# Performance work log

Hardware: AMD Instinct MI355X
Metric: run time of the kernel (lower is better)

## Reference

```python
import jax, jax.numpy as jnp
import numpy as np

B, L, D, H, DFF, MODES, ELAYERS = 64, 512, 512, 8, 2048, 32, 2
VOCAB, NUM_APP, KERNEL = 10000, 10000, 25
E = D // H


def setup_inputs() -> dict:
    key = jax.random.key(0)
    ks = jax.random.split(key, 16)
    scale = 1.0 / (D * D)  # FourierBlock weight init scale
    return {
        'x_app': jax.random.randint(ks[0], (B, L), 0, VOCAB),
        'x_time': jax.random.uniform(ks[1], (B, L), dtype=jnp.float32),
        'time_vecs': jax.random.normal(ks[2], (B, L, 24), dtype=jnp.float32),
        'targets': jax.random.randint(ks[3], (B,), 0, NUM_APP),
        'app_emb_w': jax.random.normal(ks[4], (VOCAB, D), dtype=jnp.float32) * 0.02,
        'time_w': jax.random.normal(ks[5], (D,), dtype=jnp.float32) * 0.02,
        'time_b': jnp.zeros((D,), jnp.float32),
        'Wq': jax.random.normal(ks[6], (ELAYERS, D, D), dtype=jnp.float32) * 0.02,
        'bq': jnp.zeros((ELAYERS, D), jnp.float32),
        'Wo': jax.random.normal(ks[7], (ELAYERS, D, D), dtype=jnp.float32) * 0.02,
        'bo': jnp.zeros((ELAYERS, D), jnp.float32),
        'four_wr': jax.random.uniform(ks[8], (ELAYERS, H, E, E, MODES), dtype=jnp.float32) * scale,
        'four_wi': jax.random.uniform(ks[9], (ELAYERS, H, E, E, MODES), dtype=jnp.float32) * scale,
        'conv1_w': jax.random.normal(ks[10], (ELAYERS, DFF, D), dtype=jnp.float32) * 0.02,
        'conv2_w': jax.random.normal(ks[11], (ELAYERS, D, DFF), dtype=jnp.float32) * 0.02,
        'norm_w': jnp.ones((D,), jnp.float32),
        'norm_b': jnp.zeros((D,), jnp.float32),
        'proj_w': jax.random.normal(ks[12], (NUM_APP, D + 24), dtype=jnp.float32) * 0.02,
        'proj_b': jnp.zeros((NUM_APP,), jnp.float32),
    }


def moving_avg(x):
    # edge-replicate pad by (K-1)//2 on each side, then AvgPool1d(K, stride=1)
    pad = (KERNEL - 1) // 2
    xp = jnp.pad(x, ((0, 0), (pad, pad), (0, 0)), mode='edge')  # [B, L+K-1, D]
    cs = jnp.cumsum(xp, axis=1)
    cs = jnp.concatenate([jnp.zeros_like(cs[:, :1]), cs], axis=1)
    return (cs[:, KERNEL:] - cs[:, :-KERNEL]) / KERNEL  # [B, L, D]


def series_decomp(x):
    m = moving_avg(x)
    return x - m, m


def my_layernorm(x, w, b, eps=1e-5):
    mu = jnp.mean(x, axis=-1, keepdims=True)
    var = jnp.mean((x - mu) ** 2, axis=-1, keepdims=True)
    xh = (x - mu) * jax.lax.rsqrt(var + eps) * w + b
    # my_Layernorm: subtract per-sample mean over the sequence dim
    return xh - jnp.mean(xh, axis=1, keepdims=True)


def fourier_block(q, wr, wi):
    # q: [B, L, H, E] -> [B, H, E, L]
    Bq, Lq, Hq, Eq = q.shape
    x = jnp.transpose(q, (0, 2, 3, 1))
    x_ft = jnp.fft.rfft(x, axis=-1)             # [B,H,E,L//2+1] complex64
    xs = x_ft[..., :MODES]                      # low-frequency mode selection
    w = (wr + 1j * wi).astype(xs.dtype)         # [H,E,E,M]
    out_sel = jnp.einsum('bhim,hiom->bhom', xs, w)
    out_ft = jnp.zeros((Bq, Hq, Eq, Lq // 2 + 1), dtype=xs.dtype).at[..., :MODES].set(out_sel)
    return jnp.fft.irfft(out_ft, n=Lq, axis=-1)  # [B,H,E,L]


def encoder_layer(x, Wq, bq, Wo, bo, wr, wi, c1, c2):
    Bx, Lx, Dx = x.shape
    q = (x @ Wq.T + bq).reshape(Bx, Lx, H, E)
    out = fourier_block(q, wr, wi)               # [B,H,E,L]
    # faithful to torch: out.view(B, L, -1) is a raw row-major reinterpret
    out = out.reshape(Bx, Lx, H * E)
    new_x = out @ Wo.T + bo
    x = x + new_x
    x, _ = series_decomp(x)
    y = jax.nn.relu(jnp.einsum('bld,fd->blf', x, c1))   # conv1 (1x1, no bias)
    y = jnp.einsum('blf,df->bld', y, c2)                # conv2 (1x1, no bias)
    res, _ = series_decomp(x + y)
    return res


def reference(x_app, x_time, time_vecs, targets, app_emb_w, time_w, time_b,
              Wq, bq, Wo, bo, four_wr, four_wi, conv1_w, conv2_w,
              norm_w, norm_b, proj_w, proj_b):
    x = app_emb_w[x_app] + x_time[..., None] * time_w + time_b  # [B,L,D]
    for l in range(ELAYERS):
        x = encoder_layer(x, Wq[l], bq[l], Wo[l], bo[l],
                          four_wr[l], four_wi[l], conv1_w[l], conv2_w[l])
    x = my_layernorm(x, norm_w, norm_b)
    last = x[:, -1, :]                                   # [B,D]
    out = jnp.concatenate([last, time_vecs[:, -1, :]], axis=1)  # [B,D+24]
    score = out @ proj_w.T + proj_b                      # [B,NUM_APP]
    return score  # mode='predict' returns score
```

## Files before the change

### kernel.cpp

```cpp
#include <hip/hip_runtime.h>


typedef unsigned short u16;
typedef float f32x4 __attribute__((ext_vector_type(4)));
typedef __bf16 bf16x8 __attribute__((ext_vector_type(8)));

__device__ __forceinline__ u16 f2b(float f) {
  unsigned u = __float_as_uint(f);
  return (u16)((u + 0x7FFFu + ((u >> 16) & 1u)) >> 16);
}
__device__ __forceinline__ float b2f(u16 v) {
  return __uint_as_float((unsigned)v << 16);
}
__device__ __forceinline__ f32x4 b4f(ushort4 v) {
  f32x4 r;
  r.x = b2f(v.x); r.y = b2f(v.y); r.z = b2f(v.z); r.w = b2f(v.w);
  return r;
}

__device__ __forceinline__ void gll16(const void* g, void* l) {
  __builtin_amdgcn_global_load_lds(
      (const __attribute__((address_space(1))) void*)g,
      (__attribute__((address_space(3))) void*)l, 16, 0, 0);
}

template<bool SWAP>
__device__ __forceinline__ f32x4 mfma16(bf16x8 a, bf16x8 b, f32x4 c) {
  if constexpr (SWAP)
    return __builtin_amdgcn_mfma_f32_16x16x32_bf16(b, a, c, 0, 0, 0);
  else
    return __builtin_amdgcn_mfma_f32_16x16x32_bf16(a, b, c, 0, 0, 0);
}

template<bool BIAS, bool RELU, bool RES, bool OUTBF16, bool GUARD, bool TRANS,
         bool SWZ>
__global__ __launch_bounds__(256, 3)
void k_gemm(const u16* __restrict__ A, const u16* __restrict__ B,
            const float* __restrict__ bias, const u16* __restrict__ res,
            float* __restrict__ Cf, u16* __restrict__ Cb,
            int M, int N, int K,
            long zA, long zB, long zC, int nbn, int nbm)
{
  __shared__ __align__(16) u16 sA[2][128 * 32];
  __shared__ __align__(16) u16 sB[2][128 * 32];
  const int tid = threadIdx.x;
  const int wave = tid >> 6, lane = tid & 63;
  int bn, bm;
  if (SWZ) {
    int bid = blockIdx.x;
    int xcd = bid & 7, loc = bid >> 3;
    bn = loc % nbn;
    bm = xcd * (nbm >> 3) + loc / nbn;
  } else {
    bn = blockIdx.x;
    bm = blockIdx.y;
  }
  const int bz = blockIdx.z;
  const int wm = (wave >> 1) * 64, wn = (wave & 1) * 64;

  A += (size_t)bz * zA;
  B += (size_t)bz * zB;

  const int r0 = tid >> 2;
  const int lg = tid & 3;
  const int ps = lg ^ ((r0 >> 1) & 3);
  int gmA0 = bm * 128 + r0, gmA1 = gmA0 + 64;
  int gnB0 = bn * 128 + r0, gnB1 = gnB0 + 64;
  if (GUARD) {
    gmA0 = gmA0 < M ? gmA0 : M - 1;
    gmA1 = gmA1 < M ? gmA1 : M - 1;
    gnB0 = gnB0 < N ? gnB0 : N - 1;
    gnB1 = gnB1 < N ? gnB1 : N - 1;
  }
  const size_t rb = (size_t)K * 2;
  const char* pa0 = (const char*)A + (size_t)gmA0 * rb + lg * 16;
  const char* pa1 = (const char*)A + (size_t)gmA1 * rb + lg * 16;
  const char* pb0 = (const char*)B + (size_t)gnB0 * rb + lg * 16;
  const char* pb1 = (const char*)B + (size_t)gnB1 * rb + lg * 16;
  const int w0 = r0 * 32 + ps * 8;

  f32x4 acc[4][4];
  const f32x4 z = {0.f, 0.f, 0.f, 0.f};
#pragma unroll
  for (int i = 0; i < 4; ++i)
#pragma unroll
    for (int j = 0; j < 4; ++j) acc[i][j] = z;

  const int r = lane & 15, qd = lane >> 4;
  const int pA = (qd ^ ((lane >> 1) & 3)) * 8;
  const int nk = K >> 5;

  uint4 va0, va1, vb0, vb1;
  auto gload = [&](int kt) {
    const size_t ko = (size_t)kt * 64;
    va0 = *(const uint4*)(pa0 + ko);
    va1 = *(const uint4*)(pa1 + ko);
    vb0 = *(const uint4*)(pb0 + ko);
    vb1 = *(const uint4*)(pb1 + ko);
  };

  gload(0);
  int pg = 0;
  for (int kt = 0; kt < nk; ++kt) {
    *(uint4*)&sA[pg][w0]        = va0;
    *(uint4*)&sA[pg][w0 + 2048] = va1;
    *(uint4*)&sB[pg][w0]        = vb0;
    *(uint4*)&sB[pg][w0 + 2048] = vb1;
    if (kt + 1 < nk) gload(kt + 1);
    __syncthreads();
    bf16x8 af[4], bg[4];
#pragma unroll
    for (int mi = 0; mi < 4; ++mi)
      af[mi] = *(const bf16x8*)&sA[pg][(wm + mi * 16 + r) * 32 + pA];
#pragma unroll
    for (int ni = 0; ni < 4; ++ni)
      bg[ni] = *(const bf16x8*)&sB[pg][(wn + ni * 16 + r) * 32 + pA];
#pragma unroll
    for (int mi = 0; mi < 4; ++mi)
#pragma unroll
      for (int ni = 0; ni < 4; ++ni)
        acc[mi][ni] = mfma16<!TRANS>(af[mi], bg[ni], acc[mi][ni]);
    pg ^= 1;
  }

  if (Cf) Cf += (size_t)bz * zC;
  if (Cb) Cb += (size_t)bz * zC;

  if constexpr (!TRANS) {
#pragma unroll
    for (int mi = 0; mi < 4; ++mi) {
      const int gm = bm * 128 + wm + mi * 16 + r;
      if (GUARD && gm >= M) continue;
#pragma unroll
      for (int ni = 0; ni < 4; ++ni) {
        const int gn0 = bn * 128 + wn + ni * 16 + qd * 4;
        if (GUARD && gn0 >= N) continue;
        float v[4];
        ushort4 rv;
        if (RES) rv = *(const ushort4*)&res[(size_t)gm * N + gn0];
#pragma unroll
        for (int e = 0; e < 4; ++e) {
          v[e] = acc[mi][ni][e];
          if (BIAS) v[e] += bias[gn0 + e];
          if (RES)  v[e] += b2f(e == 0 ? rv.x : e == 1 ? rv.y : e == 2 ? rv.z : rv.w);
          if (RELU) v[e] = v[e] > 0.f ? v[e] : 0.f;
        }
        if (OUTBF16) {
          ushort4 o;
          o.x = f2b(v[0]); o.y = f2b(v[1]); o.z = f2b(v[2]); o.w = f2b(v[3]);
          *(ushort4*)&Cb[(size_t)gm * N + gn0] = o;
        } else {
          float4 o = {v[0], v[1], v[2], v[3]};
          *(float4*)&Cf[(size_t)gm * N + gn0] = o;
        }
      }
    }
  } else {
#pragma unroll
    for (int ni = 0; ni < 4; ++ni) {
      const int gn = bn * 128 + wn + ni * 16 + r;
      if (GUARD && gn >= N) continue;
      const float bb = BIAS ? bias[gn] : 0.f;
#pragma unroll
      for (int mi = 0; mi < 4; ++mi) {
        const int gm0 = bm * 128 + wm + mi * 16 + qd * 4;
        if (GUARD && gm0 >= M) continue;
        float v[4];
#pragma unroll
        for (int e = 0; e < 4; ++e) {
          v[e] = acc[mi][ni][e];
          if (BIAS) v[e] += bb;
          if (RELU) v[e] = v[e] > 0.f ? v[e] : 0.f;
        }
        if (OUTBF16) {
          ushort4 o;
          o.x = f2b(v[0]); o.y = f2b(v[1]); o.z = f2b(v[2]); o.w = f2b(v[3]);
          *(ushort4*)&Cb[(size_t)gn * M + gm0] = o;
        } else {
          float4 o = {v[0], v[1], v[2], v[3]};
          *(float4*)&Cf[(size_t)gn * M + gm0] = o;
        }
      }
    }
  }
}

template<bool BIAS, bool RELU, bool RES, bool TRANS>
__global__ __launch_bounds__(512, 4)
void k_gemm3(const u16* __restrict__ A, const u16* __restrict__ B,
             const float* __restrict__ bias, const u16* __restrict__ res,
             u16* __restrict__ C, int M, int N, int K,
             int nbn, int nbm, long zA, long zC)
{
  __shared__ __align__(16) u16 sA[3][256 * 32];
  __shared__ __align__(16) u16 sB[3][128 * 32];
  const int tid = threadIdx.x;
  const int w8 = tid >> 6, lane = tid & 63;
  const int bid = blockIdx.x;
  const int xcd = bid & 7, loc = bid >> 3;
  const int mpx = (int)(gridDim.x >> 3) / nbn;
  const int mflat = xcd * mpx + loc / nbn;
  const int bn = loc % nbn;
  const int bz = mflat / nbm;
  const int bm = mflat - bz * nbm;
  const int wm = (w8 >> 1) * 64, wn = (w8 & 1) * 64;

  A += (size_t)bz * zA;

  const int r0 = tid >> 2;
  const int lg = (tid & 3) ^ ((r0 >> 1) & 3);
  const u16* pA0 = A + (size_t)(bm * 256 + r0) * K + lg * 8;
  const u16* pA1 = pA0 + (size_t)128 * K;
  const u16* pB0 = B + (size_t)(bn * 128 + r0) * K + lg * 8;
  const int la0 = w8 * 512;
  const int la1 = 4096 + w8 * 512;

  const int nk = K >> 5;

  auto stage = [&](int t, int sb) {
    const size_t ko = (size_t)t * 32;
    gll16(pA0 + ko, &sA[sb][0] + la0);
    gll16(pA1 + ko, &sA[sb][0] + la1);
    gll16(pB0 + ko, &sB[sb][0] + la0);
  };

  f32x4 acc[4][4];
  const f32x4 z = {0.f, 0.f, 0.f, 0.f};
#pragma unroll
  for (int i = 0; i < 4; ++i)
#pragma unroll
    for (int j = 0; j < 4; ++j) acc[i][j] = z;

  const int fr = lane & 15, qd = lane >> 4;
  const int pAo = ((qd ^ ((lane >> 1) & 3)) << 3);

  stage(0, 0);
  stage(1, 1);
  int cb = 0;
  for (int t = 0; t < nk; ++t) {
    if (t + 1 < nk) asm volatile("s_waitcnt vmcnt(3)" ::: "memory");
    else            asm volatile("s_waitcnt vmcnt(0)" ::: "memory");
    __builtin_amdgcn_s_barrier();
    asm volatile("" ::: "memory");
    const u16* bufA = &sA[cb][0];
    const u16* bufB = &sB[cb][0];
    bf16x8 af[4], bg[4];
#pragma unroll
    for (int i = 0; i < 4; ++i)
      af[i] = *(const bf16x8*)&bufA[(wm + i * 16 + fr) * 32 + pAo];
#pragma unroll
    for (int i = 0; i < 4; ++i)
      bg[i] = *(const bf16x8*)&bufB[(wn + i * 16 + fr) * 32 + pAo];
    if (t + 2 < nk) {
      int sb = cb + 2; if (sb >= 3) sb -= 3;
      stage(t + 2, sb);
    }
    __builtin_amdgcn_s_setprio(1);
#pragma unroll
    for (int mi = 0; mi < 4; ++mi)
#pragma unroll
      for (int ni = 0; ni < 4; ++ni)
        acc[mi][ni] = mfma16<!TRANS>(af[mi], bg[ni], acc[mi][ni]);
    __builtin_amdgcn_s_setprio(0);
    cb = (cb == 2) ? 0 : cb + 1;
  }

  C += (size_t)bz * zC;

  if constexpr (!TRANS) {
#pragma unroll
    for (int mi = 0; mi < 4; ++mi) {
      const int gm = bm * 256 + wm + mi * 16 + fr;
#pragma unroll
      for (int ni = 0; ni < 4; ++ni) {
        const int gn0 = bn * 128 + wn + ni * 16 + qd * 4;
        float v[4];
        ushort4 rv;
        if (RES) rv = *(const ushort4*)&res[(size_t)gm * N + gn0];
#pragma unroll
        for (int e = 0; e < 4; ++e) {
          v[e] = acc[mi][ni][e];
          if (BIAS) v[e] += bias[gn0 + e];
          if (RES)  v[e] += b2f(e == 0 ? rv.x : e == 1 ? rv.y : e == 2 ? rv.z : rv.w);
          if (RELU) v[e] = v[e] > 0.f ? v[e] : 0.f;
        }
        ushort4 o;
        o.x = f2b(v[0]); o.y = f2b(v[1]); o.z = f2b(v[2]); o.w = f2b(v[3]);
        *(ushort4*)&C[(size_t)gm * N + gn0] = o;
      }
    }
  } else {
#pragma unroll
    for (int ni = 0; ni < 4; ++ni) {
      const int gn = bn * 128 + wn + ni * 16 + fr;
      const float bb = BIAS ? bias[gn] : 0.f;
#pragma unroll
      for (int mi = 0; mi < 4; ++mi) {
        const int gm0 = bm * 256 + wm + mi * 16 + qd * 4;
        float v[4];
#pragma unroll
        for (int e = 0; e < 4; ++e) {
          v[e] = acc[mi][ni][e];
          if (BIAS) v[e] += bb;
          if (RELU) v[e] = v[e] > 0.f ? v[e] : 0.f;
        }
        ushort4 o;
        o.x = f2b(v[0]); o.y = f2b(v[1]); o.z = f2b(v[2]); o.w = f2b(v[3]);
        *(ushort4*)&C[(size_t)gn * M + gm0] = o;
      }
    }
  }
}

__global__ void k_basis(u16* __restrict__ dftB, u16* __restrict__ Binv)
{
  int id = blockIdx.x * 256 + threadIdx.x;
  if (id >= 32768) return;
  {
    int m = id >> 9, l = id & 511;
    int mm = m & 31;
    float ang = (float)((l * mm) & 511) * (6.283185307179586f / 512.f);
    float s, c;
    __sincosf(ang, &s, &c);
    dftB[id] = f2b(m < 32 ? c : -s);
  }
  {
    int l = id >> 6, m = id & 63;
    int mm = m & 31;
    float ang = (float)((l * mm) & 511) * (6.283185307179586f / 512.f);
    float s, c;
    __sincosf(ang, &s, &c);
    float v;
    if (m < 32) v = (m == 0 ? 1.f : 2.f) * (1.f / 512.f) * c;
    else        v = (mm == 0 ? 0.f : (-2.f / 512.f) * s);
    Binv[id] = f2b(v);
  }
}

__global__ void k_convert(const float* __restrict__ in, u16* __restrict__ out, int n)
{
  int id = blockIdx.x * 256 + threadIdx.x;
  if (id < n) out[id] = f2b(in[id]);
}

__global__ void k_convproj(const float* __restrict__ w, u16* __restrict__ o)
{
  int id = blockIdx.x * 256 + threadIdx.x;
  if (id >= 10000 * 544) return;
  int n = id / 544, k = id % 544;
  o[id] = f2b(k < 536 ? w[(size_t)n * 536 + k] : 0.f);
}

__global__ void k_transp(const float* __restrict__ wr, const float* __restrict__ wi,
                         float* __restrict__ wrT, float* __restrict__ wiT)
{
  __shared__ float tr[64 * 33], ti[64 * 33];
  int blk = blockIdx.x;
  int t = threadIdx.x;
  int lh = blk >> 6, i = blk & 63;
  const size_t src = (size_t)blk * 2048;
#pragma unroll
  for (int p = 0; p < 8; ++p) {
    int id = p * 256 + t;
    int o = id >> 5, m = id & 31;
    tr[o * 33 + m] = wr[src + id];
    ti[o * 33 + m] = wi[src + id];
  }
  __syncthreads();
#pragma unroll
  for (int p = 0; p < 8; ++p) {
    int id = p * 256 + t;
    int m = id >> 6, o = id & 63;
    size_t dst = ((size_t)(lh * 32 + m) * 64 + i) * 64 + o;
    wrT[dst] = tr[o * 33 + m];
    wiT[dst] = ti[o * 33 + m];
  }
}

__global__ void k_embed(const int* __restrict__ xapp, const float* __restrict__ xtime,
                        const float* __restrict__ emb, const float* __restrict__ tw,
                        const float* __restrict__ tb, u16* __restrict__ xb)
{
  int id = blockIdx.x * 256 + threadIdx.x;
  int j = id & 127, bl = id >> 7;
  float4 e = ((const float4*)emb)[(size_t)xapp[bl] * 128 + j];
  float t = xtime[bl];
  float4 w4 = ((const float4*)tw)[j];
  float4 b4 = ((const float4*)tb)[j];
  ushort4 o;
  o.x = f2b(e.x + t * w4.x + b4.x);
  o.y = f2b(e.y + t * w4.y + b4.y);
  o.z = f2b(e.z + t * w4.z + b4.z);
  o.w = f2b(e.w + t * w4.w + b4.w);
  ((ushort4*)xb)[id] = o;
}

__global__ __launch_bounds__(256)
void k_mix(const float* __restrict__ spec, const float* __restrict__ wrT,
           const float* __restrict__ wiT, u16* __restrict__ Ab)
{
  __shared__ float swr[4096], swi[4096];
  __shared__ float sre[4][64], sim[4][64];
  int hm = blockIdx.x;
  int bg = blockIdx.y;
  int h = hm >> 5, m = hm & 31, t = threadIdx.x;
  const float* wrb = wrT + (size_t)hm * 4096;
  const float* wib = wiT + (size_t)hm * 4096;
#pragma unroll
  for (int p = 0; p < 16; ++p) {
    int id = p * 256 + t;
    swr[id] = wrb[id];
    swi[id] = wib[id];
  }
  int o = t & 63, bsub = t >> 6;
  for (int b0 = 0; b0 < 16; b0 += 4) {
    __syncthreads();
    int b = bg * 16 + b0 + bsub;
    const float* spb = spec + (size_t)b * 32768;
    sre[bsub][o] = spb[m * 512 + h * 64 + o];
    sim[bsub][o] = spb[(32 + m) * 512 + h * 64 + o];
    __syncthreads();
    float aR = 0.f, aI = 0.f;
#pragma unroll 8
    for (int i = 0; i < 64; ++i) {
      float xr = sre[bsub][i], xi = sim[bsub][i];
      float wrv = swr[i * 64 + o], wiv = swi[i * 64 + o];
      aR += xr * wrv - xi * wiv;
      aI += xr * wiv + xi * wrv;
    }
    size_t row = (size_t)b * 512 + h * 64 + o;
    Ab[row * 64 + m] = f2b(aR);
    Ab[row * 64 + 32 + m] = f2b(aI);
  }
}

__global__ void k_decomp(const u16* __restrict__ in, u16* __restrict__ outb)
{
  int blk = blockIdx.x;
  int j = blk >> 3;
  int b = (blk & 7) + 8 * (j >> 3);
  int ck = (j & 7) * 2 + (threadIdx.x >> 7);
  int d4 = threadIdx.x & 127;
  const ushort4* xb = (const ushort4*)(in + (size_t)b * 262144) + d4;
  ushort4* ob = (ushort4*)(outb + (size_t)b * 262144) + d4;
  int l0 = ck * 32;
  f32x4 sum = {0.f, 0.f, 0.f, 0.f};
#pragma unroll
  for (int jj = -12; jj <= 12; ++jj) {
    int idx = l0 + jj;
    idx = idx < 0 ? 0 : idx;
    sum += b4f(xb[idx * 128]);
  }
#pragma unroll 4
  for (int l = l0; l < l0 + 32; ++l) {
    f32x4 xv = b4f(xb[l * 128]);
    f32x4 o = xv - sum * (1.f / 25.f);
    ushort4 ov;
    ov.x = f2b(o.x); ov.y = f2b(o.y); ov.z = f2b(o.z); ov.w = f2b(o.w);
    ob[l * 128] = ov;
    int ia = l + 13 > 511 ? 511 : l + 13;
    int ir = l - 12 < 0 ? 0 : l - 12;
    sum += b4f(xb[ia * 128]) - b4f(xb[ir * 128]);
  }
}

__global__ void k_lnstats(const u16* __restrict__ x, float* __restrict__ mu,
                          float* __restrict__ rs)
{
  int row = blockIdx.x;
  const u16* xr = x + (size_t)row * 512;
  int t = threadIdx.x;
  ushort2 p = ((const ushort2*)xr)[t];
  float v0 = b2f(p.x), v1 = b2f(p.y);
  float s = v0 + v1, ss = v0 * v0 + v1 * v1;
#pragma unroll
  for (int off = 32; off; off >>= 1) {
    s += __shfl_down(s, off);
    ss += __shfl_down(ss, off);
  }
  __shared__ float as[4], ass[4];
  if ((t & 63) == 0) { as[t >> 6] = s; ass[t >> 6] = ss; }
  __syncthreads();
  if (t == 0) {
    float S = as[0] + as[1] + as[2] + as[3];
    float SS = ass[0] + ass[1] + ass[2] + ass[3];
    float m = S * (1.f / 512.f);
    float var = SS * (1.f / 512.f) - m * m;
    mu[row] = m;
    rs[row] = rsqrtf(var + 1e-5f);
  }
}

__global__ void k_lastcat1(const u16* __restrict__ x, const float* __restrict__ mu,
                           const float* __restrict__ rs, float* __restrict__ part)
{
  int b = blockIdx.x >> 3, g = blockIdx.x & 7, t = threadIdx.x;
  const u16* xb = x + (size_t)b * 262144;
  const float* mub = mu + b * 512;
  const float* rsb = rs + b * 512;
  float a0 = 0.f, a1 = 0.f;
#pragma unroll 4
  for (int l = g * 64; l < g * 64 + 64; ++l) {
    float m = mub[l], rr = rsb[l];
    ushort2 p = ((const ushort2*)(xb + l * 512))[t];
    a0 += (b2f(p.x) - m) * rr;
    a1 += (b2f(p.y) - m) * rr;
  }
  part[((size_t)b * 8 + g) * 512 + 2 * t]     = a0;
  part[((size_t)b * 8 + g) * 512 + 2 * t + 1] = a1;
}

__global__ void k_lastcat2(const u16* __restrict__ x, const float* __restrict__ mu,
                           const float* __restrict__ rs, const float* __restrict__ part,
                           const float* __restrict__ nw, u16* __restrict__ cat)
{
  int b = blockIdx.x, t = threadIdx.x;
#pragma unroll
  for (int hh = 0; hh < 2; ++hh) {
    int d = t + hh * 256;
    float acc = 0.f;
#pragma unroll
    for (int g = 0; g < 8; ++g)
      acc += part[((size_t)b * 8 + g) * 512 + d];
    float lastv = (b2f(x[(size_t)b * 262144 + 511 * 512 + d]) - mu[b * 512 + 511])
                  * rs[b * 512 + 511];
    cat[b * 544 + d] = f2b(nw[d] * (lastv - acc * (1.f / 512.f)));
  }
}

__global__ void k_timecat(const float* __restrict__ tv, u16* __restrict__ cat)
{
  int id = blockIdx.x * 256 + threadIdx.x;
  if (id >= 2048) return;
  int b = id >> 5, j = id & 31;
  int pos = 512 + j;
  float v = (pos < 536) ? tv[((size_t)b * 512 + 511) * 24 + (pos - 512)] : 0.f;
  cat[b * 544 + pos] = f2b(v);
}

extern "C" void kernel_launch(void* const* d_in, const int* in_sizes, int n_in,
                              void* d_out, int out_size, void* d_ws, size_t ws_size,
                              hipStream_t stream)
{
  (void)in_sizes; (void)n_in; (void)out_size; (void)ws_size;
  const int*   x_app  = (const int*)  d_in[0];
  const float* x_time = (const float*)d_in[1];
  const float* tvec   = (const float*)d_in[2];
  const float* emb    = (const float*)d_in[4];
  const float* time_w = (const float*)d_in[5];
  const float* time_b = (const float*)d_in[6];
  const float* Wq     = (const float*)d_in[7];
  const float* bq     = (const float*)d_in[8];
  const float* Wo     = (const float*)d_in[9];
  const float* bo     = (const float*)d_in[10];
  const float* fwr    = (const float*)d_in[11];
  const float* fwi    = (const float*)d_in[12];
  const float* c1     = (const float*)d_in[13];
  const float* c2     = (const float*)d_in[14];
  const float* norm_w = (const float*)d_in[15];
  const float* proj_w = (const float*)d_in[17];
  const float* proj_b = (const float*)d_in[18];
  float* out = (float*)d_out;

  char* w = (char*)d_ws;
  auto alloc = [&](size_t bytes) -> char* {
    char* p = w;
    w += (bytes + 255) & ~(size_t)255;
    return p;
  };
  u16*   Cb   = (u16*)  alloc(33554432);
  u16*   YqT  = (u16*)  alloc(134217728);
  u16*   T1b  = (u16*)  alloc(33554432);
  float* S1   = (float*)alloc(8388608);
  u16*   Coef = (u16*)  alloc(4194304);
  float* wrT  = (float*)alloc(2 * 1048576 * 4);
  float* wiT  = (float*)alloc(2 * 1048576 * 4);
  u16*   wqb  = (u16*)  alloc(2 * 262144 * 2);
  u16*   wob  = (u16*)  alloc(2 * 262144 * 2);
  u16*   c1b  = (u16*)  alloc(2 * 1048576 * 2);
  u16*   c2b  = (u16*)  alloc(2 * 1048576 * 2);
  u16*   pwb  = (u16*)  alloc(10000 * 544 * 2);
  u16*   dftB = (u16*)  alloc(64 * 512 * 2);
  u16*   Binv = (u16*)  alloc(512 * 64 * 2);
  float* muB  = (float*)alloc(131072);
  float* rsB  = (float*)alloc(131072);
  float* part = (float*)alloc(64 * 8 * 512 * 4);
  u16*   cat  = (u16*)  alloc(64 * 544 * 2);

  k_basis<<<128, 256, 0, stream>>>(dftB, Binv);
  k_transp<<<1024, 256, 0, stream>>>(fwr, fwi, wrT, wiT);
  k_convert<<<2048, 256, 0, stream>>>(Wq, wqb, 524288);
  k_convert<<<2048, 256, 0, stream>>>(Wo, wob, 524288);
  k_convert<<<8192, 256, 0, stream>>>(c1, c1b, 2097152);
  k_convert<<<8192, 256, 0, stream>>>(c2, c2b, 2097152);
  k_convproj<<<21250, 256, 0, stream>>>(proj_w, pwb);
  k_embed<<<16384, 256, 0, stream>>>(x_app, x_time, emb, time_w, time_b, Cb);

  for (int l = 0; l < 2; ++l) {
    const u16* wq_l = wqb + l * 262144;
    const u16* wo_l = wob + l * 262144;
    const u16* c1_l = c1b + l * 1048576;
    const u16* c2_l = c2b + l * 1048576;

    k_gemm3<true, false, false, true>
        <<<512, 512, 0, stream>>>(
        Cb, wq_l, bq + l * 512, nullptr, YqT, 512, 512, 512,
        4, 2, 262144, 262144);
    k_gemm<false, false, false, false, true, true, false>
        <<<dim3(1, 4, 64), 256, 0, stream>>>(
        YqT, dftB, nullptr, nullptr, S1, nullptr, 512, 64, 512,
        262144, 0, 32768, 0, 0);
    k_mix<<<dim3(256, 4), 256, 0, stream>>>(
        S1, wrT + l * 1048576, wiT + l * 1048576, Coef);
    k_gemm<false, false, false, true, false, false, true>
        <<<dim3(1024, 1, 1), 256, 0, stream>>>(
        Coef, Binv, nullptr, nullptr, nullptr, YqT, 32768, 512, 64,
        0, 0, 0, 4, 256);
    k_gemm3<true, false, true, false>
        <<<512, 512, 0, stream>>>(
        YqT, wo_l, bo + l * 512, Cb, T1b, 32768, 512, 512,
        4, 128, 0, 0);
    k_decomp<<<512, 256, 0, stream>>>(T1b, Cb);
    k_gemm3<false, true, false, false>
        <<<2048, 512, 0, stream>>>(
        Cb, c1_l, nullptr, nullptr, YqT, 32768, 2048, 512,
        16, 128, 0, 0);
    k_gemm3<false, false, true, false>
        <<<512, 512, 0, stream>>>(
        YqT, c2_l, nullptr, Cb, T1b, 32768, 512, 2048,
        4, 128, 0, 0);
    k_decomp<<<512, 256, 0, stream>>>(T1b, Cb);
  }

  k_lnstats<<<32768, 256, 0, stream>>>(Cb, muB, rsB);
  k_lastcat1<<<512, 256, 0, stream>>>(Cb, muB, rsB, part);
  k_lastcat2<<<64, 256, 0, stream>>>(Cb, muB, rsB, part, norm_w, cat);
  k_timecat<<<8, 256, 0, stream>>>(tvec, cat);
  k_gemm<true, false, false, false, true, false, false>
      <<<dim3(79, 1, 1), 256, 0, stream>>>(
      cat, pwb, proj_b, nullptr, out, nullptr, 64, 10000, 544,
      0, 0, 0, 0, 0);
}
```

Baseline: 872.6 us.

## Use 4-wave GEMM blocks with 128x64 per-wave tiles and double buffering

The bf16 GEMM kernel used for the linear layers now runs 256 threads per block instead of 512, while the 256x128 block tile stays the same. Each wave now computes a 128x64 sub-tile with 32 accumulators instead of 16, which doubles register reuse of the B fragments per LDS read. The LDS pipeline drops from triple to double buffering and waits for all loads before each step, freeing shared memory but leaving less prefetch overlap. The higher register pressure and fewer waves per block may reduce latency hiding.

```diff
diff --git a/kernel.cpp b/kernel.cpp
--- a/kernel.cpp
+++ b/kernel.cpp
@@ -186,16 +186,16 @@
 }
 
 template<bool BIAS, bool RELU, bool RES, bool TRANS>
-__global__ __launch_bounds__(512, 4)
-void k_gemm3(const u16* __restrict__ A, const u16* __restrict__ B,
+__global__ __launch_bounds__(256, 3)
+void k_gemm4(const u16* __restrict__ A, const u16* __restrict__ B,
              const float* __restrict__ bias, const u16* __restrict__ res,
              u16* __restrict__ C, int M, int N, int K,
              int nbn, int nbm, long zA, long zC)
 {
-  __shared__ __align__(16) u16 sA[3][256 * 32];
-  __shared__ __align__(16) u16 sB[3][128 * 32];
+  __shared__ __align__(16) u16 sA[2][256 * 32];
+  __shared__ __align__(16) u16 sB[2][128 * 32];
   const int tid = threadIdx.x;
-  const int w8 = tid >> 6, lane = tid & 63;
+  const int w4 = tid >> 6, lane = tid & 63;
   const int bid = blockIdx.x;
   const int xcd = bid & 7, loc = bid >> 3;
   const int mpx = (int)(gridDim.x >> 3) / nbn;
@@ -203,31 +203,32 @@
   const int bn = loc % nbn;
   const int bz = mflat / nbm;
   const int bm = mflat - bz * nbm;
-  const int wm = (w8 >> 1) * 64, wn = (w8 & 1) * 64;
+  const int wm = (w4 >> 1) * 128, wn = (w4 & 1) * 64;
 
   A += (size_t)bz * zA;
 
   const int r0 = tid >> 2;
   const int lg = (tid & 3) ^ ((r0 >> 1) & 3);
   const u16* pA0 = A + (size_t)(bm * 256 + r0) * K + lg * 8;
-  const u16* pA1 = pA0 + (size_t)128 * K;
   const u16* pB0 = B + (size_t)(bn * 128 + r0) * K + lg * 8;
-  const int la0 = w8 * 512;
-  const int la1 = 4096 + w8 * 512;
+  const int wb = w4 * 512;
 
   const int nk = K >> 5;
 
   auto stage = [&](int t, int sb) {
     const size_t ko = (size_t)t * 32;
-    gll16(pA0 + ko, &sA[sb][0] + la0);
-    gll16(pA1 + ko, &sA[sb][0] + la1);
-    gll16(pB0 + ko, &sB[sb][0] + la0);
+#pragma unroll
+    for (int j = 0; j < 4; ++j)
+      gll16(pA0 + (size_t)(j * 64) * K + ko, &sA[sb][j * 2048 + wb]);
+#pragma unroll
+    for (int j = 0; j < 2; ++j)
+      gll16(pB0 + (size_t)(j * 64) * K + ko, &sB[sb][j * 2048 + wb]);
   };
 
-  f32x4 acc[4][4];
+  f32x4 acc[8][4];
   const f32x4 z = {0.f, 0.f, 0.f, 0.f};
 #pragma unroll
-  for (int i = 0; i < 4; ++i)
+  for (int i = 0; i < 8; ++i)
 #pragma unroll
     for (int j = 0; j < 4; ++j) acc[i][j] = z;
 
@@ -235,41 +236,35 @@
   const int pAo = ((qd ^ ((lane >> 1) & 3)) << 3);
 
   stage(0, 0);
-  stage(1, 1);
-  int cb = 0;
   for (int t = 0; t < nk; ++t) {
-    if (t + 1 < nk) asm volatile("s_waitcnt vmcnt(3)" ::: "memory");
-    else            asm volatile("s_waitcnt vmcnt(0)" ::: "memory");
+    const int cb = t & 1;
+    asm volatile("s_waitcnt vmcnt(0)" ::: "memory");
     __builtin_amdgcn_s_barrier();
     asm volatile("" ::: "memory");
     const u16* bufA = &sA[cb][0];
     const u16* bufB = &sB[cb][0];
-    bf16x8 af[4], bg[4];
-#pragma unroll
-    for (int i = 0; i < 4; ++i)
+    bf16x8 af[8], bg[4];
+#pragma unroll
+    for (int i = 0; i < 8; ++i)
       af[i] = *(const bf16x8*)&bufA[(wm + i * 16 + fr) * 32 + pAo];
 #pragma unroll
     for (int i = 0; i < 4; ++i)
       bg[i] = *(const bf16x8*)&bufB[(wn + i * 16 + fr) * 32 + pAo];
-    if (t + 2 < nk) {
-      int sb = cb + 2; if (sb >= 3) sb -= 3;
-      stage(t + 2, sb);
-    }
+    if (t + 1 < nk) stage(t + 1, cb ^ 1);
     __builtin_amdgcn_s_setprio(1);
 #pragma unroll
-    for (int mi = 0; mi < 4; ++mi)
+    for (int mi = 0; mi < 8; ++mi)
 #pragma unroll
       for (int ni = 0; ni < 4; ++ni)
         acc[mi][ni] = mfma16<!TRANS>(af[mi], bg[ni], acc[mi][ni]);
     __builtin_amdgcn_s_setprio(0);
-    cb = (cb == 2) ? 0 : cb + 1;
   }
 
   C += (size_t)bz * zC;
 
   if constexpr (!TRANS) {
 #pragma unroll
-    for (int mi = 0; mi < 4; ++mi) {
+    for (int mi = 0; mi < 8; ++mi) {
       const int gm = bm * 256 + wm + mi * 16 + fr;
 #pragma unroll
       for (int ni = 0; ni < 4; ++ni) {
@@ -295,7 +290,7 @@
       const int gn = bn * 128 + wn + ni * 16 + fr;
       const float bb = BIAS ? bias[gn] : 0.f;
 #pragma unroll
-      for (int mi = 0; mi < 4; ++mi) {
+      for (int mi = 0; mi < 8; ++mi) {
         const int gm0 = bm * 256 + wm + mi * 16 + qd * 4;
         float v[4];
 #pragma unroll
@@ -602,8 +597,8 @@
     const u16* c1_l = c1b + l * 1048576;
     const u16* c2_l = c2b + l * 1048576;
 
-    k_gemm3<true, false, false, true>
-        <<<512, 512, 0, stream>>>(
+    k_gemm4<true, false, false, true>
+        <<<512, 256, 0, stream>>>(
         Cb, wq_l, bq + l * 512, nullptr, YqT, 512, 512, 512,
         4, 2, 262144, 262144);
     k_gemm<false, false, false, false, true, true, false>
@@ -616,17 +611,17 @@
         <<<dim3(1024, 1, 1), 256, 0, stream>>>(
         Coef, Binv, nullptr, nullptr, nullptr, YqT, 32768, 512, 64,
         0, 0, 0, 4, 256);
-    k_gemm3<true, false, true, false>
-        <<<512, 512, 0, stream>>>(
+    k_gemm4<true, false, true, false>
+        <<<512, 256, 0, stream>>>(
         YqT, wo_l, bo + l * 512, Cb, T1b, 32768, 512, 512,
         4, 128, 0, 0);
     k_decomp<<<512, 256, 0, stream>>>(T1b, Cb);
-    k_gemm3<false, true, false, false>
-        <<<2048, 512, 0, stream>>>(
+    k_gemm4<false, true, false, false>
+        <<<2048, 256, 0, stream>>>(
         Cb, c1_l, nullptr, nullptr, YqT, 32768, 2048, 512,
         16, 128, 0, 0);
-    k_gemm3<false, false, true, false>
-        <<<512, 512, 0, stream>>>(
+    k_gemm4<false, false, true, false>
+        <<<512, 256, 0, stream>>>(
         YqT, c2_l, nullptr, Cb, T1b, 32768, 512, 2048,
         4, 128, 0, 0);
     k_decomp<<<512, 256, 0, stream>>>(T1b, Cb);
```

After: 2.312 ms. +164.9%, slower.
